# Optimization experiments

Hardware: AMD Instinct MI355X
Metric: run time of the kernel (lower is better)

The kernel has to match this reference:

```python
import jax, jax.numpy as jnp
import numpy as np

# init kwargs (constants)
P = 1            # chamfer_distance_p
WEIGHT = 1.0
XYZ_UNIT = 0.1


def setup_inputs() -> dict:
    key = jax.random.key(0)
    k1, k2 = jax.random.split(key)
    B, N, M, D = 16, 4096, 4096, 3
    pred = jax.random.normal(k1, (B, N, D), dtype=jnp.float32)
    gt = jax.random.normal(k2, (B, M, D), dtype=jnp.float32)
    return {"pred": pred, "gt": gt}


def _chamfer(x, y, p):
    x2 = jnp.sum(x * x, axis=-1)                       # [B, N]
    y2 = jnp.sum(y * y, axis=-1)                       # [B, M]
    xy = jnp.einsum('bnd,bmd->bnm', x, y)              # [B, N, M]
    sq = jnp.maximum(x2[:, :, None] + y2[:, None, :] - 2.0 * xy, 0.0)
    dist = jnp.sqrt(sq)                                # torch.norm(x-y, dim=3)
    if p != 1:
        dist = dist ** p
    x_loss = jnp.mean(jnp.min(dist, axis=2), axis=1)   # [B]
    y_loss = jnp.mean(jnp.min(dist, axis=1), axis=1)   # [B]
    return jnp.mean(x_loss + y_loss)                   # scalar (reduce=True)


def reference(pred, gt):
    # HelperPointLoss.forward with reduce_over_batch=True, loss_name='chamfer_distance'
    loss = _chamfer(pred, gt, P)
    # info['helper_loss'] = loss (detached); info['helper_cderr'] = p=1 chamfer * xyz_unit
    cderr = _chamfer(pred, gt, 1) * XYZ_UNIT
    return (WEIGHT * loss, loss, cderr)
```

## Files before the change

### kernel.cpp

```cpp
#include <hip/hip_runtime.h>
#include <hip/hip_fp16.h>

typedef __attribute__((ext_vector_type(8)))  _Float16 half8;
typedef __attribute__((ext_vector_type(16))) float    f32x16;

#define B_   16
#define NPTS 4096

constexpr int BLK  = 256;
constexpr int WV   = 4;
constexpr int QPW  = 32;
constexpr int QPB  = WV * QPW;
constexpr int NQC  = NPTS / QPB;
constexpr int RT   = 1024;
constexpr int NR   = NPTS / RT;
constexpr int TPR  = RT / 32;
constexpr int NBLK = 2 * B_ * NQC;

__device__ __forceinline__ float min3f(float a, float b, float c) {
    return fminf(fminf(a, b), c);
}

__global__ __launch_bounds__(BLK, 4) void chamfer_mfma(
        const float* __restrict__ pred, const float* __restrict__ gt,
        float* __restrict__ accum, unsigned* __restrict__ counter,
        float* __restrict__ out) {
    const int qc  = blockIdx.x;
    const int b   = blockIdx.y;
    const int dir = blockIdx.z;
    const float* qsrc = dir ? gt   : pred;
    const float* tsrc = dir ? pred : gt;

    __shared__ uint4 sh[RT];
    __shared__ float ps[WV];

    const int tid  = threadIdx.x;
    const int lane = tid & 63;
    const int wv   = tid >> 6;
    const int m    = lane & 31;

    const float* qp = qsrc + (b * NPTS + qc * QPB + wv * QPW + m) * 3;
    __half hqx = __float2half(qp[0]);
    __half hqy = __float2half(qp[1]);
    __half hqz = __float2half(qp[2]);
    float fqx = __half2float(hqx), fqy = __half2float(hqy), fqz = __half2float(hqz);
    const float q2 = fmaf(fqx, fqx, fmaf(fqy, fqy, fqz * fqz));
    uint4 bu;
    bu.x = (unsigned)__half_as_ushort(hqx) | ((unsigned)__half_as_ushort(hqy) << 16);
    bu.y = (unsigned)__half_as_ushort(hqz) | (0x3C00u << 16);
    bu.z = 0x3C00u;
    bu.w = 0u;
    const half8 bfrag = __builtin_bit_cast(half8, bu);

    f32x16 zero;
#pragma unroll
    for (int i = 0; i < 16; ++i) zero[i] = 0.0f;

    float mn = 1e30f;

    for (int r = 0; r < NR; ++r) {
        if (r) __syncthreads();
        const float* tp = tsrc + (b * NPTS + r * RT) * 3;
#pragma unroll
        for (int k = 0; k < RT / BLK; ++k) {
            int j = k * BLK + tid;
            __half hx = __float2half(tp[3 * j + 0]);
            __half hy = __float2half(tp[3 * j + 1]);
            __half hz = __float2half(tp[3 * j + 2]);
            float fx = __half2float(hx), fy = __half2float(hy), fz = __half2float(hz);
            float g2 = fmaf(fx, fx, fmaf(fy, fy, fz * fz));
            __half ax = __float2half(-2.0f * fx);
            __half ay = __float2half(-2.0f * fy);
            __half az = __float2half(-2.0f * fz);
            __half g2hi = __float2half(g2);
            __half g2lo = __float2half(g2 - __half2float(g2hi));
            uint4 w;
            w.x = (unsigned)__half_as_ushort(ax) | ((unsigned)__half_as_ushort(ay) << 16);
            w.y = (unsigned)__half_as_ushort(az) | ((unsigned)__half_as_ushort(g2hi) << 16);
            w.z = (unsigned)__half_as_ushort(g2lo);
            w.w = 0u;
            sh[j] = w;
        }
        __syncthreads();

#pragma unroll 8
        for (int t = 0; t < TPR; ++t) {
            uint4 au = sh[t * 32 + m];
            half8 afrag = __builtin_bit_cast(half8, au);
            f32x16 d = __builtin_amdgcn_mfma_f32_32x32x16_f16(afrag, bfrag, zero, 0, 0, 0);
            float m0 = min3f(d[0],  d[1],  d[2]);
            float m1 = min3f(d[3],  d[4],  d[5]);
            float m2 = min3f(d[6],  d[7],  d[8]);
            float m3 = min3f(d[9],  d[10], d[11]);
            float m4 = min3f(d[12], d[13], d[14]);
            float n0 = min3f(m0, m1, m2);
            float n1 = min3f(m3, m4, d[15]);
            mn = min3f(mn, n0, n1);
        }
    }

    float v  = fminf(mn, __shfl_xor(mn, 32));
    float dd = fmaxf(fmaf(0.5f, v, q2), 0.0f);
    float s  = sqrtf(dd);
#pragma unroll
    for (int off = 32; off; off >>= 1) s += __shfl_xor(s, off);
    if (lane == 0) ps[wv] = 0.5f * s;
    __syncthreads();

    if (tid == 0) {
        float bs = ps[0] + ps[1] + ps[2] + ps[3];
        atomicAdd(accum, bs);
        __threadfence();
        if (atomicAdd(counter, 1u) == NBLK - 1) {
            float total = atomicAdd(accum, 0.0f);
            float loss  = total * (1.0f / (float)(B_ * NPTS));
            out[0] = loss;
            out[1] = loss;
            out[2] = 0.1f * loss;
        }
    }
}

extern "C" void kernel_launch(void* const* d_in, const int* in_sizes, int n_in,
                              void* d_out, int out_size, void* d_ws, size_t ws_size,
                              hipStream_t stream) {
    const float* pred = (const float*)d_in[0];
    const float* gt   = (const float*)d_in[1];
    float*    out     = (float*)d_out;
    float*    accum   = (float*)d_ws;
    unsigned* counter = (unsigned*)d_ws + 1;

    hipMemsetAsync(d_ws, 0, 8, stream);
    chamfer_mfma<<<dim3(NQC, B_, 2), BLK, 0, stream>>>(pred, gt, accum, counter, out);
}
```

Baseline: 91.48 us.

## Split target range across waves in larger blocks and stage all targets once

Blocks grow to 1024 threads (16 waves). Each group of four waves shares one set of 32 queries and splits the 4096 targets four ways. All target points are converted and staged into LDS in one pass, which removes the chunked staging loop and its repeated barriers. Per-query partial minima are combined across the four target splits through shared memory before the sqrt and sum. The cost is 64KB of LDS per block, which caps blocks per CU. The launch-bounds hint of 8 blocks of 1024 threads is unreachable and may push the compiler to tighten register limits.

```diff
diff --git a/kernel.cpp b/kernel.cpp
--- a/kernel.cpp
+++ b/kernel.cpp
@@ -7,21 +7,22 @@
 #define B_   16
 #define NPTS 4096
 
-constexpr int BLK  = 256;
-constexpr int WV   = 4;
+constexpr int BLK  = 1024;
+constexpr int WV   = 16;
 constexpr int QPW  = 32;
-constexpr int QPB  = WV * QPW;
+constexpr int TSPL = 4;
+constexpr int QG   = WV / TSPL;
+constexpr int QPB  = QG * QPW;
 constexpr int NQC  = NPTS / QPB;
-constexpr int RT   = 1024;
-constexpr int NR   = NPTS / RT;
-constexpr int TPR  = RT / 32;
+constexpr int TPS  = NPTS / TSPL;
+constexpr int TPW  = TPS / 32;
 constexpr int NBLK = 2 * B_ * NQC;
 
 __device__ __forceinline__ float min3f(float a, float b, float c) {
     return fminf(fminf(a, b), c);
 }
 
-__global__ __launch_bounds__(BLK, 4) void chamfer_mfma(
+__global__ __launch_bounds__(BLK, 8) void chamfer_mfma(
         const float* __restrict__ pred, const float* __restrict__ gt,
         float* __restrict__ accum, unsigned* __restrict__ counter,
         float* __restrict__ out) {
@@ -31,15 +32,18 @@
     const float* qsrc = dir ? gt   : pred;
     const float* tsrc = dir ? pred : gt;
 
-    __shared__ uint4 sh[RT];
-    __shared__ float ps[WV];
+    __shared__ uint4 sh[NPTS];
+    __shared__ float sred[WV][QPW];
+    __shared__ float ps[2];
 
     const int tid  = threadIdx.x;
     const int lane = tid & 63;
     const int wv   = tid >> 6;
     const int m    = lane & 31;
+    const int qg   = wv >> 2;
+    const int ts   = wv & 3;
 
-    const float* qp = qsrc + (b * NPTS + qc * QPB + wv * QPW + m) * 3;
+    const float* qp = qsrc + (b * NPTS + qc * QPB + qg * QPW + m) * 3;
     __half hqx = __float2half(qp[0]);
     __half hqy = __float2half(qp[1]);
     __half hqz = __float2half(qp[2]);
@@ -56,59 +60,65 @@
 #pragma unroll
     for (int i = 0; i < 16; ++i) zero[i] = 0.0f;
 
+    const float* tp = tsrc + b * NPTS * 3;
+#pragma unroll
+    for (int k = 0; k < NPTS / BLK; ++k) {
+        int j = k * BLK + tid;
+        __half hx = __float2half(tp[3 * j + 0]);
+        __half hy = __float2half(tp[3 * j + 1]);
+        __half hz = __float2half(tp[3 * j + 2]);
+        float fx = __half2float(hx), fy = __half2float(hy), fz = __half2float(hz);
+        float g2 = fmaf(fx, fx, fmaf(fy, fy, fz * fz));
+        __half ax = __float2half(-2.0f * fx);
+        __half ay = __float2half(-2.0f * fy);
+        __half az = __float2half(-2.0f * fz);
+        __half g2hi = __float2half(g2);
+        __half g2lo = __float2half(g2 - __half2float(g2hi));
+        uint4 w;
+        w.x = (unsigned)__half_as_ushort(ax) | ((unsigned)__half_as_ushort(ay) << 16);
+        w.y = (unsigned)__half_as_ushort(az) | ((unsigned)__half_as_ushort(g2hi) << 16);
+        w.z = (unsigned)__half_as_ushort(g2lo);
+        w.w = 0u;
+        sh[j] = w;
+    }
+    __syncthreads();
+
     float mn = 1e30f;
-
-    for (int r = 0; r < NR; ++r) {
-        if (r) __syncthreads();
-        const float* tp = tsrc + (b * NPTS + r * RT) * 3;
-#pragma unroll
-        for (int k = 0; k < RT / BLK; ++k) {
-            int j = k * BLK + tid;
-            __half hx = __float2half(tp[3 * j + 0]);
-            __half hy = __float2half(tp[3 * j + 1]);
-            __half hz = __float2half(tp[3 * j + 2]);
-            float fx = __half2float(hx), fy = __half2float(hy), fz = __half2float(hz);
-            float g2 = fmaf(fx, fx, fmaf(fy, fy, fz * fz));
-            __half ax = __float2half(-2.0f * fx);
-            __half ay = __float2half(-2.0f * fy);
-            __half az = __float2half(-2.0f * fz);
-            __half g2hi = __float2half(g2);
-            __half g2lo = __float2half(g2 - __half2float(g2hi));
-            uint4 w;
-            w.x = (unsigned)__half_as_ushort(ax) | ((unsigned)__half_as_ushort(ay) << 16);
-            w.y = (unsigned)__half_as_ushort(az) | ((unsigned)__half_as_ushort(g2hi) << 16);
-            w.z = (unsigned)__half_as_ushort(g2lo);
-            w.w = 0u;
-            sh[j] = w;
-        }
-        __syncthreads();
-
 #pragma unroll 8
-        for (int t = 0; t < TPR; ++t) {
-            uint4 au = sh[t * 32 + m];
-            half8 afrag = __builtin_bit_cast(half8, au);
-            f32x16 d = __builtin_amdgcn_mfma_f32_32x32x16_f16(afrag, bfrag, zero, 0, 0, 0);
-            float m0 = min3f(d[0],  d[1],  d[2]);
-            float m1 = min3f(d[3],  d[4],  d[5]);
-            float m2 = min3f(d[6],  d[7],  d[8]);
-            float m3 = min3f(d[9],  d[10], d[11]);
-            float m4 = min3f(d[12], d[13], d[14]);
-            float n0 = min3f(m0, m1, m2);
-            float n1 = min3f(m3, m4, d[15]);
-            mn = min3f(mn, n0, n1);
-        }
+    for (int t = 0; t < TPW; ++t) {
+        uint4 au = sh[ts * TPS + t * 32 + m];
+        half8 afrag = __builtin_bit_cast(half8, au);
+        f32x16 d = __builtin_amdgcn_mfma_f32_32x32x16_f16(afrag, bfrag, zero, 0, 0, 0);
+        float m0 = min3f(d[0],  d[1],  d[2]);
+        float m1 = min3f(d[3],  d[4],  d[5]);
+        float m2 = min3f(d[6],  d[7],  d[8]);
+        float m3 = min3f(d[9],  d[10], d[11]);
+        float m4 = min3f(d[12], d[13], d[14]);
+        float n0 = min3f(m0, m1, m2);
+        float n1 = min3f(m3, m4, d[15]);
+        mn = min3f(mn, n0, n1);
     }
 
     float v  = fminf(mn, __shfl_xor(mn, 32));
     float dd = fmaxf(fmaf(0.5f, v, q2), 0.0f);
-    float s  = sqrtf(dd);
+    if (lane < 32) sred[wv][m] = dd;
+    __syncthreads();
+
+    float s = 0.0f;
+    if (wv < 2) {
+        const int g  = tid >> 5;
+        const int mm = tid & 31;
+        float d0 = fminf(sred[g * 4 + 0][mm], sred[g * 4 + 1][mm]);
+        float d1 = fminf(sred[g * 4 + 2][mm], sred[g * 4 + 3][mm]);
+        s = sqrtf(fminf(d0, d1));
 #pragma unroll
-    for (int off = 32; off; off >>= 1) s += __shfl_xor(s, off);
-    if (lane == 0) ps[wv] = 0.5f * s;
+        for (int off = 32; off; off >>= 1) s += __shfl_xor(s, off);
+        if (lane == 0) ps[wv] = s;
+    }
     __syncthreads();
 
     if (tid == 0) {
-        float bs = ps[0] + ps[1] + ps[2] + ps[3];
+        float bs = ps[0] + ps[1];
         atomicAdd(accum, bs);
         __threadfence();
         if (atomicAdd(counter, 1u) == NBLK - 1) {
```

After: 88.67 us. 1.03x faster.
